# Optimization experiments

Measured on AMD Instinct MI355X. Metric: run time of the kernel, lower is better.

## Reference

```python
import jax, jax.numpy as jnp
import numpy as np

NEG_SLOPE = 0.2

def gat_conv(x, edge_index, W, a_src, a_dst, bias, heads, channels):
    # PyG GATConv (add_self_loops=False, dropout off in eval)
    N = x.shape[0]
    h = (x @ W).reshape(N, heads, channels)               # [N,H,C]
    src, dst = edge_index[0], edge_index[1]
    e_src = jnp.einsum('nhc,hc->nh', h, a_src)            # [N,H]
    e_dst = jnp.einsum('nhc,hc->nh', h, a_dst)
    e = jax.nn.leaky_relu(e_src[src] + e_dst[dst], NEG_SLOPE)  # [E,H]
    # softmax over incoming edges of each destination node
    m = jax.ops.segment_max(e, dst, num_segments=N)       # [N,H]
    ex = jnp.exp(e - m[dst])
    s = jax.ops.segment_sum(ex, dst, num_segments=N)
    alpha = ex / (s[dst] + 1e-16)                         # [E,H]
    msg = h[src] * alpha[:, :, None]                      # [E,H,C]
    out = jax.ops.segment_sum(msg, dst, num_segments=N)   # [N,H,C]
    return out.reshape(N, heads * channels) + bias


def setup_inputs() -> dict:
    key = jax.random.key(0)
    ks = jax.random.split(key, 12)
    N, E, SED, HID, H, F_OUT = 20000, 320000, 768, 128, 4, 128
    return {
        'x': jax.random.normal(ks[0], (N, SED), jnp.float32),
        'edge_index': jax.random.randint(ks[1], (2, E), 0, N, jnp.int32),
        'sentence_embedding': jax.random.normal(ks[2], (SED,), jnp.float32),
        'W1': jax.random.normal(ks[3], (2 * SED, H * HID), jnp.float32) * 0.02,
        'a1_src': jax.random.normal(ks[4], (H, HID), jnp.float32) * 0.1,
        'a1_dst': jax.random.normal(ks[5], (H, HID), jnp.float32) * 0.1,
        'b1': jax.random.normal(ks[6], (H * HID,), jnp.float32) * 0.02,
        'W2': jax.random.normal(ks[7], (H * HID, F_OUT), jnp.float32) * 0.02,
        'a2_src': jax.random.normal(ks[8], (1, F_OUT), jnp.float32) * 0.1,
        'a2_dst': jax.random.normal(ks[9], (1, F_OUT), jnp.float32) * 0.1,
        'b2': jax.random.normal(ks[10], (F_OUT,), jnp.float32) * 0.02,
    }


def reference(x, edge_index, sentence_embedding, W1, a1_src, a1_dst, b1, W2, a2_src, a2_dst, b2):
    N = x.shape[0]
    sent = jnp.broadcast_to(sentence_embedding[None, :], (N, sentence_embedding.shape[0]))
    h = jnp.concatenate([x, sent], axis=1)                # [N, 2*SED]
    h = gat_conv(h, edge_index, W1, a1_src, a1_dst, b1, heads=4, channels=128)
    h = jax.nn.elu(h)
    out = gat_conv(h, edge_index, W2, a2_src, a2_dst, b2, heads=1, channels=128)
    return out
```

## Files before the change

kernel.cpp:

```cpp
#include <hip/hip_runtime.h>
#include <cstdint>
#include <cstddef>

#define NSLOPE 0.2f

typedef __attribute__((ext_vector_type(8))) short bf16x8;
typedef __attribute__((ext_vector_type(4))) float f32x4;
typedef __attribute__((ext_vector_type(2))) float f32x2;
typedef unsigned short ushort_t;

__device__ inline ushort_t f2bf(float f) {
    union { float f; unsigned u; } v; v.f = f;
    unsigned u = v.u;
    unsigned r = (u + 0x7fffu + ((u >> 16) & 1u)) >> 16;
    return (ushort_t)r;
}
__device__ inline f32x2 unpack2(unsigned u) {
    union { unsigned u; float f; } lo, hi;
    lo.u = u << 16;
    hi.u = u & 0xffff0000u;
    f32x2 r; r.x = lo.f; r.y = hi.f;
    return r;
}
__device__ inline float leaky(float v) { return (v > 0.f) ? v : NSLOPE * v; }
__device__ inline float sel4(float4 q, bool b1, bool b2) {
    return b2 ? (b1 ? q.w : q.z) : (b1 ? q.y : q.x);
}

__global__ __launch_bounds__(256) void prep_kernel(
    const float* __restrict__ x, ushort_t* __restrict__ x_bf16, size_t nx,
    const float* __restrict__ W1, ushort_t* __restrict__ W1T,
    const float* __restrict__ W2, ushort_t* __restrict__ W2T,
    const float* __restrict__ sent, float* __restrict__ svec_part,
    int* __restrict__ indeg, int N, int nbCast, int nbZero)
{
    __shared__ float tile[32][33];
    int bid = blockIdx.x;
    int tid = threadIdx.x;
    if (bid < nbCast) {
        size_t i = ((size_t)bid * 256 + tid) * 8;
        if (i < nx) {
            float4 v0 = *(const float4*)(x + i);
            float4 v1 = *(const float4*)(x + i + 4);
            ushort_t r[8] = { f2bf(v0.x), f2bf(v0.y), f2bf(v0.z), f2bf(v0.w),
                              f2bf(v1.x), f2bf(v1.y), f2bf(v1.z), f2bf(v1.w) };
            *(uint4*)(x_bf16 + i) = *(uint4*)r;
        }
        return;
    }
    bid -= nbCast;
    if (bid < 384) {
        int k0 = (bid % 24) * 32, n0 = (bid / 24) * 32;
        int tx = tid & 31, ty = tid >> 5;
#pragma unroll
        for (int i = 0; i < 4; ++i)
            tile[ty + i * 8][tx] = W1[(size_t)(k0 + ty + i * 8) * 512 + n0 + tx];
        __syncthreads();
#pragma unroll
        for (int i = 0; i < 4; ++i)
            W1T[(size_t)(n0 + ty + i * 8) * 768 + k0 + tx] = f2bf(tile[tx][ty + i * 8]);
        return;
    }
    bid -= 384;
    if (bid < 64) {
        int k0 = (bid % 16) * 32, n0 = (bid / 16) * 32;
        int tx = tid & 31, ty = tid >> 5;
#pragma unroll
        for (int i = 0; i < 4; ++i)
            tile[ty + i * 8][tx] = W2[(size_t)(k0 + ty + i * 8) * 128 + n0 + tx];
        __syncthreads();
#pragma unroll
        for (int i = 0; i < 4; ++i)
            W2T[(size_t)(n0 + ty + i * 8) * 512 + k0 + tx] = f2bf(tile[tx][ty + i * 8]);
        return;
    }
    bid -= 64;
    if (bid < 16) {
        int cb = bid & 1, kb = bid >> 1;
        int c = cb * 256 + tid;
        int k0 = kb * 96;
        float acc = 0.f;
#pragma unroll 8
        for (int k = k0; k < k0 + 96; ++k)
            acc += sent[k] * W1[(size_t)(768 + k) * 512 + c];
        svec_part[kb * 512 + c] = acc;
        return;
    }
    bid -= 16;
    {
        int i = bid * 256 + tid;
        if (i < N) indeg[i] = 0;
    }
}

__device__ inline void async_copy16(const void* g, void* l) {
    __builtin_amdgcn_global_load_lds(
        (const __attribute__((address_space(1))) unsigned int*)g,
        (__attribute__((address_space(3))) unsigned int*)l, 16, 0, 0);
}

__global__ __launch_bounds__(256) void mfma_gemm_kernel(
    const ushort_t* __restrict__ A,
    const ushort_t* __restrict__ BT,
    const float* __restrict__ bias,
    ushort_t* __restrict__ Cb,
    const float* __restrict__ asrc,
    const float* __restrict__ adst,
    float* __restrict__ e_src,
    float* __restrict__ e_dst,
    int eStride,
    int M, int K, int Nc)
{
    __shared__ __align__(16) ushort_t lA[3][64 * 32];
    __shared__ __align__(16) ushort_t lB[3][128 * 32];
    __shared__ float e_lds[64][2][2];
    const int tid = threadIdx.x;
    const int wave = tid >> 6;
    const int lane = tid & 63;

    const int hh = blockIdx.y * gridDim.x + blockIdx.x;
    const int xcd = hh & 7;
    const int slot = hh >> 3;
    const int by = xcd + 8 * (slot / gridDim.x);
    const int bx = slot % gridDim.x;

    const int col0 = bx * 128;
    const int row0 = by * 64;
    const int wm = (wave & 1) * 32;
    const int wn = (wave >> 1) * 64;
    const int q = lane >> 4;
    const int ml = lane & 15;

    f32x4 acc[2][4] = {};

    const int rA = tid >> 2;
    const int gA = (tid & 3) ^ ((rA >> 1) & 3);
    int rowS[2], gS[2];
#pragma unroll
    for (int i = 0; i < 2; ++i) {
        int p = wave * 128 + i * 64 + lane;
        int r = p >> 2, s = p & 3;
        rowS[i] = r;
        gS[i] = s ^ ((r >> 1) & 3);
    }

    auto stage = [&](int k0, int buf) {
        {
            int ga = min(row0 + rA, M - 1);
            async_copy16(A + (size_t)ga * K + k0 + gA * 8,
                         &lA[buf][(size_t)(wave * 64) * 8]);
        }
#pragma unroll
        for (int i = 0; i < 2; ++i) {
            int pbs = wave * 128 + i * 64;
            async_copy16(BT + (size_t)(col0 + rowS[i]) * K + k0 + gS[i] * 8,
                         &lB[buf][(size_t)pbs * 8]);
        }
    };

    const int nt = K >> 5;
    stage(0, 0);
    if (nt > 1) {
        stage(32, 1);
        asm volatile("s_waitcnt vmcnt(3)\n\ts_barrier" ::: "memory");
    } else {
        asm volatile("s_waitcnt vmcnt(0)\n\ts_barrier" ::: "memory");
    }

    for (int t = 0; t < nt; ++t) {
        const int pb = t % 3;
        if (t + 2 < nt) stage((t + 2) << 5, (t + 2) % 3);
        bf16x8 af[2], bfr[4];
#pragma unroll
        for (int tt = 0; tt < 2; ++tt) {
            int m = wm + tt * 16 + ml;
            af[tt] = *(const bf16x8*)&lA[pb][(size_t)(m * 4 + (q ^ ((m >> 1) & 3))) * 8];
        }
#pragma unroll
        for (int tt = 0; tt < 4; ++tt) {
            int n = wn + tt * 16 + ml;
            bfr[tt] = *(const bf16x8*)&lB[pb][(size_t)(n * 4 + (q ^ ((n >> 1) & 3))) * 8];
        }
#pragma unroll
        for (int tm = 0; tm < 2; ++tm)
#pragma unroll
            for (int tn = 0; tn < 4; ++tn)
                acc[tm][tn] = __builtin_amdgcn_mfma_f32_16x16x32_bf16(
                    af[tm], bfr[tn], acc[tm][tn], 0, 0, 0);
        if (t + 2 < nt)
            asm volatile("s_waitcnt vmcnt(3) lgkmcnt(0)\n\ts_barrier" ::: "memory");
        else if (t + 1 < nt)
            asm volatile("s_waitcnt vmcnt(0) lgkmcnt(0)\n\ts_barrier" ::: "memory");
    }

    float es_acc[2][4] = {};
    float ed_acc[2][4] = {};
#pragma unroll
    for (int tm = 0; tm < 2; ++tm) {
        int rbase = row0 + wm + tm * 16 + q * 4;
#pragma unroll
        for (int tn = 0; tn < 4; ++tn) {
            int col = col0 + wn + tn * 16 + ml;
            float bb = bias ? bias[col] : 0.f;
            float av = asrc[col];
            float dv = adst[col];
#pragma unroll
            for (int r = 0; r < 4; ++r) {
                int row = rbase + r;
                float val = acc[tm][tn][r] + bb;
                if (row < M)
                    Cb[(size_t)row * Nc + col] = f2bf(val);
                es_acc[tm][r] += val * av;
                ed_acc[tm][r] += val * dv;
            }
        }
    }
    const int colhalf = wave >> 1;
#pragma unroll
    for (int tm = 0; tm < 2; ++tm) {
#pragma unroll
        for (int r = 0; r < 4; ++r) {
            float es = es_acc[tm][r], ed2 = ed_acc[tm][r];
#pragma unroll
            for (int st = 1; st < 16; st <<= 1) {
                es += __shfl_xor(es, st);
                ed2 += __shfl_xor(ed2, st);
            }
            if (ml == 0) {
                int rl = wm + tm * 16 + q * 4 + r;
                e_lds[rl][colhalf][0] = es;
                e_lds[rl][colhalf][1] = ed2;
            }
        }
    }
    __syncthreads();
    if (tid < 64) {
        int row = row0 + tid;
        if (row < M) {
            float es = e_lds[tid][0][0] + e_lds[tid][1][0];
            float ed2 = e_lds[tid][0][1] + e_lds[tid][1][1];
            e_src[(size_t)row * eStride + bx] = es;
            e_dst[(size_t)row * eStride + bx] = ed2;
        }
    }
}

__global__ void count_kernel(const int* __restrict__ ei, int* __restrict__ indeg, int E) {
    int e = blockIdx.x * blockDim.x + threadIdx.x;
    if (e < E) atomicAdd(&indeg[ei[E + e]], 1);
}

__global__ __launch_bounds__(1024) void scan_kernel(const int* __restrict__ indeg,
                                                    int* __restrict__ offsets,
                                                    int* __restrict__ cursor,
                                                    const float* __restrict__ svec_part,
                                                    float* __restrict__ svec, int N) {
    __shared__ int partial[1024];
    int tid = threadIdx.x;
    if (tid < 512) {
        float s = 0.f;
#pragma unroll
        for (int kb = 0; kb < 8; ++kb) s += svec_part[kb * 512 + tid];
        svec[tid] = s;
    }
    int per = (N + 1023) / 1024;
    int start = tid * per;
    int end = min(start + per, N);
    int sum = 0;
    if (start + per <= N && (per & 3) == 0) {
        for (int i = 0; i < per; i += 4) {
            int4 v = *(const int4*)(indeg + start + i);
            sum += v.x + v.y + v.z + v.w;
        }
    } else {
        for (int i = start; i < end; ++i) sum += indeg[i];
    }
    partial[tid] = sum;
    __syncthreads();
    for (int st = 1; st < 1024; st <<= 1) {
        int v = (tid >= st) ? partial[tid - st] : 0;
        __syncthreads();
        partial[tid] += v;
        __syncthreads();
    }
    int run = (tid == 0) ? 0 : partial[tid - 1];
    if (start + per <= N && (per & 3) == 0) {
        for (int i = 0; i < per; i += 4) {
            int4 v = *(const int4*)(indeg + start + i);
            int4 o;
            o.x = run;
            o.y = o.x + v.x;
            o.z = o.y + v.y;
            o.w = o.z + v.z;
            run = o.w + v.w;
            *(int4*)(offsets + start + i) = o;
            *(int4*)(cursor + start + i) = o;
        }
    } else {
        for (int i = start; i < end; ++i) {
            offsets[i] = run; cursor[i] = run;
            run += indeg[i];
        }
    }
    if (tid == 1023) offsets[N] = run;
}

__global__ void scatter_kernel(const int* __restrict__ ei, int* __restrict__ cursor,
                               int* __restrict__ csr_src, int E) {
    int e = blockIdx.x * blockDim.x + threadIdx.x;
    if (e < E) {
        int d = ei[E + e];
        int p = atomicAdd(&cursor[d], 1);
        csr_src[p] = ei[e];
    }
}

__global__ __launch_bounds__(256) void gather1_kernel(
    const ushort_t* __restrict__ h1b, const float* __restrict__ e_src,
    const float* __restrict__ e_dst, const int* __restrict__ offsets,
    const int* __restrict__ csr_src, const float* __restrict__ bias,
    ushort_t* __restrict__ outb, int N)
{
    const int lane = threadIdx.x & 63;
    const int wid0 = blockIdx.x * 4 + (threadIdx.x >> 6);
    const int nw = gridDim.x * 4;

    const int h = lane >> 4;
    const bool b1 = (h & 1), b2 = (h & 2);
    const ushort_t* hp = h1b + lane * 8;
    const int c = lane * 8;
    float bias0 = bias[c],     bias1 = bias[c + 1], bias2 = bias[c + 2],
          bias3 = bias[c + 3], bias4 = bias[c + 4], bias5 = bias[c + 5],
          bias6 = bias[c + 6], bias7 = bias[c + 7];

    for (int node = __builtin_amdgcn_readfirstlane(wid0); node < N;
         node = __builtin_amdgcn_readfirstlane(node + nw)) {
        int beg = offsets[node], end = offsets[node + 1];
        float4 ed = *(const float4*)&e_dst[node * 4];
        float edh = sel4(ed, b1, b2);

        f32x2 acc[4] = {};
        float s = 0.f;

        int j = beg;
        const int nb = (end - beg) >> 2;

        int4 ia, ib;
        float4 qa0, qa1, qa2, qa3, qb0, qb1, qb2, qb3;
        uint4 ua0, ua1, ua2, ua3, ub0, ub1, ub2, ub3;

        auto load4 = [&](int jj, int4& ix,
                         float4& q0, float4& q1, float4& q2, float4& q3,
                         uint4& u0, uint4& u1, uint4& u2, uint4& u3) {
            ix.x = csr_src[jj];     ix.y = csr_src[jj + 1];
            ix.z = csr_src[jj + 2]; ix.w = csr_src[jj + 3];
            q0 = *(const float4*)&e_src[ix.x * 4];
            q1 = *(const float4*)&e_src[ix.y * 4];
            q2 = *(const float4*)&e_src[ix.z * 4];
            q3 = *(const float4*)&e_src[ix.w * 4];
            u0 = *(const uint4*)&hp[(size_t)ix.x * 512];
            u1 = *(const uint4*)&hp[(size_t)ix.y * 512];
            u2 = *(const uint4*)&hp[(size_t)ix.z * 512];
            u3 = *(const uint4*)&hp[(size_t)ix.w * 512];
        };
        auto cons4 = [&](const float4& q0, const float4& q1,
                         const float4& q2, const float4& q3,
                         const uint4& u0, const uint4& u1,
                         const uint4& u2, const uint4& u3) {
            float w0 = __expf(leaky(sel4(q0, b1, b2) + edh));
            float w1 = __expf(leaky(sel4(q1, b1, b2) + edh));
            float w2 = __expf(leaky(sel4(q2, b1, b2) + edh));
            float w3 = __expf(leaky(sel4(q3, b1, b2) + edh));
            s += (w0 + w1) + (w2 + w3);
            f32x2 wv;
            wv.x = w0; wv.y = w0;
            acc[0] += unpack2(u0.x) * wv; acc[1] += unpack2(u0.y) * wv;
            acc[2] += unpack2(u0.z) * wv; acc[3] += unpack2(u0.w) * wv;
            wv.x = w1; wv.y = w1;
            acc[0] += unpack2(u1.x) * wv; acc[1] += unpack2(u1.y) * wv;
            acc[2] += unpack2(u1.z) * wv; acc[3] += unpack2(u1.w) * wv;
            wv.x = w2; wv.y = w2;
            acc[0] += unpack2(u2.x) * wv; acc[1] += unpack2(u2.y) * wv;
            acc[2] += unpack2(u2.z) * wv; acc[3] += unpack2(u2.w) * wv;
            wv.x = w3; wv.y = w3;
            acc[0] += unpack2(u3.x) * wv; acc[1] += unpack2(u3.y) * wv;
            acc[2] += unpack2(u3.z) * wv; acc[3] += unpack2(u3.w) * wv;
        };

        if (nb > 0) {
            load4(j, ia, qa0, qa1, qa2, qa3, ua0, ua1, ua2, ua3); j += 4;
            int b = 1;
            for (; b + 1 < nb; b += 2) {
                load4(j, ib, qb0, qb1, qb2, qb3, ub0, ub1, ub2, ub3); j += 4;
                cons4(qa0, qa1, qa2, qa3, ua0, ua1, ua2, ua3);
                load4(j, ia, qa0, qa1, qa2, qa3, ua0, ua1, ua2, ua3); j += 4;
                cons4(qb0, qb1, qb2, qb3, ub0, ub1, ub2, ub3);
            }
            if (b < nb) {
                load4(j, ib, qb0, qb1, qb2, qb3, ub0, ub1, ub2, ub3); j += 4;
                cons4(qa0, qa1, qa2, qa3, ua0, ua1, ua2, ua3);
                cons4(qb0, qb1, qb2, qb3, ub0, ub1, ub2, ub3);
            } else {
                cons4(qa0, qa1, qa2, qa3, ua0, ua1, ua2, ua3);
            }
        }
        for (; j < end; ++j) {
            int s0 = csr_src[j];
            float4 q0 = *(const float4*)&e_src[s0 * 4];
            float w0 = __expf(leaky(sel4(q0, b1, b2) + edh));
            s += w0;
            uint4 u0 = *(const uint4*)&hp[(size_t)s0 * 512];
            f32x2 wv; wv.x = w0; wv.y = w0;
            acc[0] += unpack2(u0.x) * wv; acc[1] += unpack2(u0.y) * wv;
            acc[2] += unpack2(u0.z) * wv; acc[3] += unpack2(u0.w) * wv;
        }
        float rs = 1.f / (s + 1e-16f);
        ushort_t o[8];
        float r0, r1;
        r0 = acc[0].x * rs + bias0; r1 = acc[0].y * rs + bias1;
        r0 = (r0 > 0.f) ? r0 : (__expf(r0) - 1.f);
        r1 = (r1 > 0.f) ? r1 : (__expf(r1) - 1.f);
        o[0] = f2bf(r0); o[1] = f2bf(r1);
        r0 = acc[1].x * rs + bias2; r1 = acc[1].y * rs + bias3;
        r0 = (r0 > 0.f) ? r0 : (__expf(r0) - 1.f);
        r1 = (r1 > 0.f) ? r1 : (__expf(r1) - 1.f);
        o[2] = f2bf(r0); o[3] = f2bf(r1);
        r0 = acc[2].x * rs + bias4; r1 = acc[2].y * rs + bias5;
        r0 = (r0 > 0.f) ? r0 : (__expf(r0) - 1.f);
        r1 = (r1 > 0.f) ? r1 : (__expf(r1) - 1.f);
        o[4] = f2bf(r0); o[5] = f2bf(r1);
        r0 = acc[3].x * rs + bias6; r1 = acc[3].y * rs + bias7;
        r0 = (r0 > 0.f) ? r0 : (__expf(r0) - 1.f);
        r1 = (r1 > 0.f) ? r1 : (__expf(r1) - 1.f);
        o[6] = f2bf(r0); o[7] = f2bf(r1);
        *(uint4*)&outb[(size_t)node * 512 + c] = *(uint4*)o;
    }
}

__global__ __launch_bounds__(256) void gather2_kernel(
    const ushort_t* __restrict__ h2b, const float* __restrict__ e_src,
    const float* __restrict__ e_dst, const int* __restrict__ offsets,
    const int* __restrict__ csr_src, const float* __restrict__ bias,
    float* __restrict__ out, int N)
{
    const int lane = threadIdx.x & 63;
    const int wid0 = blockIdx.x * 4 + (threadIdx.x >> 6);
    const int nw = gridDim.x * 4;

    const ushort_t* hp = h2b + lane * 2;
    float biasA = bias[lane * 2], biasB = bias[lane * 2 + 1];

    for (int node = __builtin_amdgcn_readfirstlane(wid0); node < N;
         node = __builtin_amdgcn_readfirstlane(node + nw)) {
        int beg = offsets[node], end = offsets[node + 1];
        float ed = e_dst[node];

        f32x2 acc = { 0.f, 0.f };
        float s = 0.f;

        int j = beg;
        const int nb = (end - beg) >> 2;

        int4 ia, ib;
        float fa0, fa1, fa2, fa3, fb0, fb1, fb2, fb3;
        unsigned ua0, ua1, ua2, ua3, ub0, ub1, ub2, ub3;

        auto load4 = [&](int jj, int4& ix,
                         float& f0, float& f1, float& f2, float& f3,
                         unsigned& u0, unsigned& u1, unsigned& u2, unsigned& u3) {
            ix.x = csr_src[jj];     ix.y = csr_src[jj + 1];
            ix.z = csr_src[jj + 2]; ix.w = csr_src[jj + 3];
            f0 = e_src[ix.x]; f1 = e_src[ix.y];
            f2 = e_src[ix.z]; f3 = e_src[ix.w];
            u0 = *(const unsigned*)&hp[(size_t)ix.x * 128];
            u1 = *(const unsigned*)&hp[(size_t)ix.y * 128];
            u2 = *(const unsigned*)&hp[(size_t)ix.z * 128];
            u3 = *(const unsigned*)&hp[(size_t)ix.w * 128];
        };
        auto cons4 = [&](float f0, float f1, float f2, float f3,
                         unsigned u0, unsigned u1, unsigned u2, unsigned u3) {
            float w0 = __expf(leaky(f0 + ed));
            float w1 = __expf(leaky(f1 + ed));
            float w2 = __expf(leaky(f2 + ed));
            float w3 = __expf(leaky(f3 + ed));
            s += (w0 + w1) + (w2 + w3);
            f32x2 w0v = { w0, w0 }, w1v = { w1, w1 }, w2v = { w2, w2 }, w3v = { w3, w3 };
            acc += unpack2(u0) * w0v;
            acc += unpack2(u1) * w1v;
            acc += unpack2(u2) * w2v;
            acc += unpack2(u3) * w3v;
        };

        if (nb > 0) {
            load4(j, ia, fa0, fa1, fa2, fa3, ua0, ua1, ua2, ua3); j += 4;
            int b = 1;
            for (; b + 1 < nb; b += 2) {
                load4(j, ib, fb0, fb1, fb2, fb3, ub0, ub1, ub2, ub3); j += 4;
                cons4(fa0, fa1, fa2, fa3, ua0, ua1, ua2, ua3);
                load4(j, ia, fa0, fa1, fa2, fa3, ua0, ua1, ua2, ua3); j += 4;
                cons4(fb0, fb1, fb2, fb3, ub0, ub1, ub2, ub3);
            }
            if (b < nb) {
                load4(j, ib, fb0, fb1, fb2, fb3, ub0, ub1, ub2, ub3); j += 4;
                cons4(fa0, fa1, fa2, fa3, ua0, ua1, ua2, ua3);
                cons4(fb0, fb1, fb2, fb3, ub0, ub1, ub2, ub3);
            } else {
                cons4(fa0, fa1, fa2, fa3, ua0, ua1, ua2, ua3);
            }
        }
        for (; j < end; ++j) {
            int s0 = csr_src[j];
            float w0 = __expf(leaky(e_src[s0] + ed));
            s += w0;
            unsigned u0 = *(const unsigned*)&hp[(size_t)s0 * 128];
            f32x2 w0v = { w0, w0 };
            acc += unpack2(u0) * w0v;
        }
        float rs = 1.f / (s + 1e-16f);
        float2 o = make_float2(acc.x * rs + biasA, acc.y * rs + biasB);
        *(float2*)&out[(size_t)node * 128 + lane * 2] = o;
    }
}

extern "C" void kernel_launch(void* const* d_in, const int* in_sizes, int n_in,
                              void* d_out, int out_size, void* d_ws, size_t ws_size,
                              hipStream_t stream) {
    const float* x      = (const float*)d_in[0];
    const int*   ei     = (const int*)  d_in[1];
    const float* sent   = (const float*)d_in[2];
    const float* W1     = (const float*)d_in[3];
    const float* a1_src = (const float*)d_in[4];
    const float* a1_dst = (const float*)d_in[5];
    const float* b1     = (const float*)d_in[6];
    const float* W2     = (const float*)d_in[7];
    const float* a2_src = (const float*)d_in[8];
    const float* a2_dst = (const float*)d_in[9];
    const float* b2     = (const float*)d_in[10];
    float* out = (float*)d_out;

    const int N = in_sizes[0] / 768;
    const int E = in_sizes[1] / 2;

    char* p = (char*)d_ws;
    auto carve = [&](size_t bytes) {
        char* q = p;
        p += (bytes + 255) & ~(size_t)255;
        return q;
    };
    ushort_t* h1b = (ushort_t*)carve((size_t)N * 512 * 2);
    char* shared_region = carve((size_t)N * 768 * 2);
    ushort_t* x_bf16 = (ushort_t*)shared_region;
    ushort_t* h_elu_b = (ushort_t*)shared_region;
    ushort_t* h2b = (ushort_t*)carve((size_t)N * 128 * 2);
    ushort_t* W1T = (ushort_t*)carve((size_t)512 * 768 * 2);
    ushort_t* W2T = (ushort_t*)carve((size_t)128 * 512 * 2);
    float* svec_part = (float*)carve(8 * 512 * 4);
    float* svec   = (float*)carve(512 * 4);
    float* e_src1 = (float*)carve((size_t)N * 4 * 4);
    float* e_dst1 = (float*)carve((size_t)N * 4 * 4);
    float* e_src2 = (float*)carve((size_t)N * 4);
    float* e_dst2 = (float*)carve((size_t)N * 4);
    int*   indeg  = (int*)carve((size_t)N * 4);
    int*   offs   = (int*)carve((size_t)(N + 1) * 4);
    int*   cursor = (int*)carve((size_t)N * 4);
    int*   csrsrc = (int*)carve((size_t)E * 4);

    size_t nx = (size_t)N * 768;
    int nbCast = (int)((nx / 8 + 255) / 256);
    int nbZero = (N + 255) / 256;
    int nbPrep = nbCast + 384 + 64 + 16 + nbZero;

    prep_kernel<<<nbPrep, 256, 0, stream>>>(x, x_bf16, nx, W1, W1T, W2, W2T,
                                            sent, svec_part, indeg, N, nbCast, nbZero);
    count_kernel<<<(E + 255) / 256, 256, 0, stream>>>(ei, indeg, E);
    scan_kernel<<<1, 1024, 0, stream>>>(indeg, offs, cursor, svec_part, svec, N);
    scatter_kernel<<<(E + 255) / 256, 256, 0, stream>>>(ei, cursor, csrsrc, E);

    int nyPad = (((N + 63) / 64) + 7) & ~7;

    mfma_gemm_kernel<<<dim3(4, nyPad), 256, 0, stream>>>(
        x_bf16, W1T, svec, h1b, a1_src, a1_dst, e_src1, e_dst1, 4, N, 768, 512);

    gather1_kernel<<<2048, 256, 0, stream>>>(
        h1b, e_src1, e_dst1, offs, csrsrc, b1, h_elu_b, N);

    mfma_gemm_kernel<<<dim3(1, nyPad), 256, 0, stream>>>(
        h_elu_b, W2T, nullptr, h2b, a2_src, a2_dst, e_src2, e_dst2, 1, N, 512, 128);

    gather2_kernel<<<2048, 256, 0, stream>>>(
        h2b, e_src2, e_dst2, offs, csrsrc, b2, out, N);
}
```

Before: 282.8 us.

## Merge prep, count, scan, scatter into one cooperative kernel with grid syncs

Replaces the four preprocessing launches (cast/transpose prep, indegree count, single-block scan, CSR scatter) with one cooperative kernel of 1024 blocks that separates the phases with grid.sync(). The scan becomes a two-level block-sum scan distributed across the grid instead of one 1024-thread block. The goal is to remove launch gaps and the serial single-block scan. In exchange it adds five grid-wide barriers, a serial per-block offset write done by thread 0, and the svec reduction is now 2 blocks doing a 768-long loop. It also depends on all 1024 blocks being co-resident.

```diff
diff --git a/kernel.cpp b/kernel.cpp
--- a/kernel.cpp
+++ b/kernel.cpp
@@ -1,8 +1,12 @@
 #include <hip/hip_runtime.h>
+#include <hip/hip_cooperative_groups.h>
 #include <cstdint>
 #include <cstddef>
 
+namespace cg = cooperative_groups;
+
 #define NSLOPE 0.2f
+#define BUILD_NB 1024
 
 typedef __attribute__((ext_vector_type(8))) short bf16x8;
 typedef __attribute__((ext_vector_type(4))) float f32x4;
@@ -27,69 +31,133 @@
     return b2 ? (b1 ? q.w : q.z) : (b1 ? q.y : q.x);
 }
 
-__global__ __launch_bounds__(256) void prep_kernel(
+__global__ __launch_bounds__(256, 4) void build_kernel(
     const float* __restrict__ x, ushort_t* __restrict__ x_bf16, size_t nx,
     const float* __restrict__ W1, ushort_t* __restrict__ W1T,
     const float* __restrict__ W2, ushort_t* __restrict__ W2T,
-    const float* __restrict__ sent, float* __restrict__ svec_part,
-    int* __restrict__ indeg, int N, int nbCast, int nbZero)
+    const float* __restrict__ sent, float* __restrict__ svec,
+    const int* __restrict__ ei, int E,
+    int* __restrict__ indeg, int* __restrict__ offsets,
+    int* __restrict__ cursor, int* __restrict__ csr_src,
+    int* __restrict__ blockSums, int N)
 {
+    cg::grid_group grid = cg::this_grid();
     __shared__ float tile[32][33];
-    int bid = blockIdx.x;
-    int tid = threadIdx.x;
-    if (bid < nbCast) {
-        size_t i = ((size_t)bid * 256 + tid) * 8;
-        if (i < nx) {
+    __shared__ int sdata[256];
+    const int tid = threadIdx.x;
+    const int bid = blockIdx.x;
+    const size_t gsize = (size_t)BUILD_NB * 256;
+
+    if (bid < 384) {
+        int k0 = (bid % 24) * 32, n0 = (bid / 24) * 32;
+        int tx = tid & 31, ty = tid >> 5;
+#pragma unroll
+        for (int i = 0; i < 4; ++i)
+            tile[ty + i * 8][tx] = W1[(size_t)(k0 + ty + i * 8) * 512 + n0 + tx];
+        __syncthreads();
+#pragma unroll
+        for (int i = 0; i < 4; ++i)
+            W1T[(size_t)(n0 + ty + i * 8) * 768 + k0 + tx] = f2bf(tile[tx][ty + i * 8]);
+    } else if (bid < 448) {
+        int b2 = bid - 384;
+        int k0 = (b2 % 16) * 32, n0 = (b2 / 16) * 32;
+        int tx = tid & 31, ty = tid >> 5;
+#pragma unroll
+        for (int i = 0; i < 4; ++i)
+            tile[ty + i * 8][tx] = W2[(size_t)(k0 + ty + i * 8) * 128 + n0 + tx];
+        __syncthreads();
+#pragma unroll
+        for (int i = 0; i < 4; ++i)
+            W2T[(size_t)(n0 + ty + i * 8) * 512 + k0 + tx] = f2bf(tile[tx][ty + i * 8]);
+    } else if (bid < 450) {
+        int c = (bid - 448) * 256 + tid;
+        float acc = 0.f;
+#pragma unroll 8
+        for (int k = 0; k < 768; ++k)
+            acc += sent[k] * W1[(size_t)(768 + k) * 512 + c];
+        svec[c] = acc;
+    }
+    {
+        size_t nvec = nx >> 3;
+        for (size_t v = (size_t)bid * 256 + tid; v < nvec; v += gsize) {
+            size_t i = v * 8;
             float4 v0 = *(const float4*)(x + i);
             float4 v1 = *(const float4*)(x + i + 4);
             ushort_t r[8] = { f2bf(v0.x), f2bf(v0.y), f2bf(v0.z), f2bf(v0.w),
                               f2bf(v1.x), f2bf(v1.y), f2bf(v1.z), f2bf(v1.w) };
             *(uint4*)(x_bf16 + i) = *(uint4*)r;
         }
-        return;
-    }
-    bid -= nbCast;
-    if (bid < 384) {
-        int k0 = (bid % 24) * 32, n0 = (bid / 24) * 32;
-        int tx = tid & 31, ty = tid >> 5;
-#pragma unroll
-        for (int i = 0; i < 4; ++i)
-            tile[ty + i * 8][tx] = W1[(size_t)(k0 + ty + i * 8) * 512 + n0 + tx];
+    }
+    for (int i = bid * 256 + tid; i < N; i += (int)gsize) indeg[i] = 0;
+
+    grid.sync();
+
+    for (int e = bid * 256 + tid; e < E; e += (int)gsize)
+        atomicAdd(&indeg[ei[E + e]], 1);
+
+    grid.sync();
+
+    const int per = (N + BUILD_NB - 1) / BUILD_NB;
+    const int start = bid * per;
+    const int endn = min(start + per, N);
+    {
+        int v = 0;
+        for (int i = start + tid; i < endn; i += 256) v += indeg[i];
+        sdata[tid] = v;
         __syncthreads();
-#pragma unroll
-        for (int i = 0; i < 4; ++i)
-            W1T[(size_t)(n0 + ty + i * 8) * 768 + k0 + tx] = f2bf(tile[tx][ty + i * 8]);
-        return;
-    }
-    bid -= 384;
-    if (bid < 64) {
-        int k0 = (bid % 16) * 32, n0 = (bid / 16) * 32;
-        int tx = tid & 31, ty = tid >> 5;
-#pragma unroll
-        for (int i = 0; i < 4; ++i)
-            tile[ty + i * 8][tx] = W2[(size_t)(k0 + ty + i * 8) * 128 + n0 + tx];
+        for (int st = 128; st >= 1; st >>= 1) {
+            if (tid < st) sdata[tid] += sdata[tid + st];
+            __syncthreads();
+        }
+        if (tid == 0) blockSums[bid] = sdata[0];
+    }
+
+    grid.sync();
+
+    if (bid == 0) {
+        int loc[BUILD_NB / 256];
+        int base = tid * (BUILD_NB / 256);
+        int sum = 0;
+#pragma unroll
+        for (int i = 0; i < BUILD_NB / 256; ++i) {
+            loc[i] = blockSums[base + i];
+            sum += loc[i];
+        }
+        sdata[tid] = sum;
         __syncthreads();
-#pragma unroll
-        for (int i = 0; i < 4; ++i)
-            W2T[(size_t)(n0 + ty + i * 8) * 512 + k0 + tx] = f2bf(tile[tx][ty + i * 8]);
-        return;
-    }
-    bid -= 64;
-    if (bid < 16) {
-        int cb = bid & 1, kb = bid >> 1;
-        int c = cb * 256 + tid;
-        int k0 = kb * 96;
-        float acc = 0.f;
-#pragma unroll 8
-        for (int k = k0; k < k0 + 96; ++k)
-            acc += sent[k] * W1[(size_t)(768 + k) * 512 + c];
-        svec_part[kb * 512 + c] = acc;
-        return;
-    }
-    bid -= 16;
-    {
-        int i = bid * 256 + tid;
-        if (i < N) indeg[i] = 0;
+        for (int st = 1; st < 256; st <<= 1) {
+            int val = (tid >= st) ? sdata[tid - st] : 0;
+            __syncthreads();
+            sdata[tid] += val;
+            __syncthreads();
+        }
+        int run = (tid == 0) ? 0 : sdata[tid - 1];
+#pragma unroll
+        for (int i = 0; i < BUILD_NB / 256; ++i) {
+            int t = loc[i];
+            blockSums[base + i] = run;
+            run += t;
+        }
+    }
+
+    grid.sync();
+
+    if (tid == 0 && start < N) {
+        int run = blockSums[bid];
+        for (int i = start; i < endn; ++i) {
+            offsets[i] = run;
+            cursor[i] = run;
+            run += indeg[i];
+        }
+        if (endn == N) offsets[N] = run;
+    }
+
+    grid.sync();
+
+    for (int e = bid * 256 + tid; e < E; e += (int)gsize) {
+        int d = ei[E + e];
+        int p = atomicAdd(&cursor[d], 1);
+        csr_src[p] = ei[e];
     }
 }
 
@@ -242,76 +310,6 @@
             e_src[(size_t)row * eStride + bx] = es;
             e_dst[(size_t)row * eStride + bx] = ed2;
         }
-    }
-}
-
-__global__ void count_kernel(const int* __restrict__ ei, int* __restrict__ indeg, int E) {
-    int e = blockIdx.x * blockDim.x + threadIdx.x;
-    if (e < E) atomicAdd(&indeg[ei[E + e]], 1);
-}
-
-__global__ __launch_bounds__(1024) void scan_kernel(const int* __restrict__ indeg,
-                                                    int* __restrict__ offsets,
-                                                    int* __restrict__ cursor,
-                                                    const float* __restrict__ svec_part,
-                                                    float* __restrict__ svec, int N) {
-    __shared__ int partial[1024];
-    int tid = threadIdx.x;
-    if (tid < 512) {
-        float s = 0.f;
-#pragma unroll
-        for (int kb = 0; kb < 8; ++kb) s += svec_part[kb * 512 + tid];
-        svec[tid] = s;
-    }
-    int per = (N + 1023) / 1024;
-    int start = tid * per;
-    int end = min(start + per, N);
-    int sum = 0;
-    if (start + per <= N && (per & 3) == 0) {
-        for (int i = 0; i < per; i += 4) {
-            int4 v = *(const int4*)(indeg + start + i);
-            sum += v.x + v.y + v.z + v.w;
-        }
-    } else {
-        for (int i = start; i < end; ++i) sum += indeg[i];
-    }
-    partial[tid] = sum;
-    __syncthreads();
-    for (int st = 1; st < 1024; st <<= 1) {
-        int v = (tid >= st) ? partial[tid - st] : 0;
-        __syncthreads();
-        partial[tid] += v;
-        __syncthreads();
-    }
-    int run = (tid == 0) ? 0 : partial[tid - 1];
-    if (start + per <= N && (per & 3) == 0) {
-        for (int i = 0; i < per; i += 4) {
-            int4 v = *(const int4*)(indeg + start + i);
-            int4 o;
-            o.x = run;
-            o.y = o.x + v.x;
-            o.z = o.y + v.y;
-            o.w = o.z + v.z;
-            run = o.w + v.w;
-            *(int4*)(offsets + start + i) = o;
-            *(int4*)(cursor + start + i) = o;
-        }
-    } else {
-        for (int i = start; i < end; ++i) {
-            offsets[i] = run; cursor[i] = run;
-            run += indeg[i];
-        }
-    }
-    if (tid == 1023) offsets[N] = run;
-}
-
-__global__ void scatter_kernel(const int* __restrict__ ei, int* __restrict__ cursor,
-                               int* __restrict__ csr_src, int E) {
-    int e = blockIdx.x * blockDim.x + threadIdx.x;
-    if (e < E) {
-        int d = ei[E + e];
-        int p = atomicAdd(&cursor[d], 1);
-        csr_src[p] = ei[e];
     }
 }
 
@@ -554,7 +552,6 @@
     ushort_t* h2b = (ushort_t*)carve((size_t)N * 128 * 2);
     ushort_t* W1T = (ushort_t*)carve((size_t)512 * 768 * 2);
     ushort_t* W2T = (ushort_t*)carve((size_t)128 * 512 * 2);
-    float* svec_part = (float*)carve(8 * 512 * 4);
     float* svec   = (float*)carve(512 * 4);
     float* e_src1 = (float*)carve((size_t)N * 4 * 4);
     float* e_dst1 = (float*)carve((size_t)N * 4 * 4);
@@ -564,17 +561,19 @@
     int*   offs   = (int*)carve((size_t)(N + 1) * 4);
     int*   cursor = (int*)carve((size_t)N * 4);
     int*   csrsrc = (int*)carve((size_t)E * 4);
+    int*   blockSums = (int*)carve(BUILD_NB * 4);
 
     size_t nx = (size_t)N * 768;
-    int nbCast = (int)((nx / 8 + 255) / 256);
-    int nbZero = (N + 255) / 256;
-    int nbPrep = nbCast + 384 + 64 + 16 + nbZero;
-
-    prep_kernel<<<nbPrep, 256, 0, stream>>>(x, x_bf16, nx, W1, W1T, W2, W2T,
-                                            sent, svec_part, indeg, N, nbCast, nbZero);
-    count_kernel<<<(E + 255) / 256, 256, 0, stream>>>(ei, indeg, E);
-    scan_kernel<<<1, 1024, 0, stream>>>(indeg, offs, cursor, svec_part, svec, N);
-    scatter_kernel<<<(E + 255) / 256, 256, 0, stream>>>(ei, cursor, csrsrc, E);
+    int E_ = E, N_ = N;
+
+    void* bargs[] = { (void*)&x, (void*)&x_bf16, (void*)&nx,
+                      (void*)&W1, (void*)&W1T, (void*)&W2, (void*)&W2T,
+                      (void*)&sent, (void*)&svec,
+                      (void*)&ei, (void*)&E_,
+                      (void*)&indeg, (void*)&offs, (void*)&cursor,
+                      (void*)&csrsrc, (void*)&blockSums, (void*)&N_ };
+    hipLaunchCooperativeKernel((void*)build_kernel, dim3(BUILD_NB), dim3(256),
+                               bargs, 0, stream);
 
     int nyPad = (((N + 63) / 64) + 7) & ~7;
 
```

Result: slower. 922.1 us (+226.0%).

## Shard layer-1 gather across 8 column slices per block group

Applied to the files above, without the earlier changes.

The layer-1 gather kernel now splits each node's 512 output columns into 8 shards selected by blockIdx, so each wave handles 64 columns with one bf16 element per lane instead of the full row with 8 elements per lane. The intent is to raise parallelism and cut per-thread register pressure by dropping the hand-written software pipeline. In exchange, each edge's index and attention score are loaded and exponentiated 8 times (once per shard), and h loads shrink to 2-byte scalar accesses, which may waste memory transactions. Behaviour depends on the grid size being a multiple of 8, which is set in host code that is not shown.

```diff
diff --git a/kernel.cpp b/kernel.cpp
--- a/kernel.cpp
+++ b/kernel.cpp
@@ -14,6 +14,10 @@
     unsigned u = v.u;
     unsigned r = (u + 0x7fffu + ((u >> 16) & 1u)) >> 16;
     return (ushort_t)r;
+}
+__device__ inline float bf2f(ushort_t u) {
+    union { unsigned u; float f; } v; v.u = ((unsigned)u) << 16;
+    return v.f;
 }
 __device__ inline f32x2 unpack2(unsigned u) {
     union { unsigned u; float f; } lo, hi;
@@ -23,9 +27,6 @@
     return r;
 }
 __device__ inline float leaky(float v) { return (v > 0.f) ? v : NSLOPE * v; }
-__device__ inline float sel4(float4 q, bool b1, bool b2) {
-    return b2 ? (b1 ? q.w : q.z) : (b1 ? q.y : q.x);
-}
 
 __global__ __launch_bounds__(256) void prep_kernel(
     const float* __restrict__ x, ushort_t* __restrict__ x_bf16, size_t nx,
@@ -322,118 +323,43 @@
     ushort_t* __restrict__ outb, int N)
 {
     const int lane = threadIdx.x & 63;
-    const int wid0 = blockIdx.x * 4 + (threadIdx.x >> 6);
-    const int nw = gridDim.x * 4;
-
-    const int h = lane >> 4;
-    const bool b1 = (h & 1), b2 = (h & 2);
-    const ushort_t* hp = h1b + lane * 8;
-    const int c = lane * 8;
-    float bias0 = bias[c],     bias1 = bias[c + 1], bias2 = bias[c + 2],
-          bias3 = bias[c + 3], bias4 = bias[c + 4], bias5 = bias[c + 5],
-          bias6 = bias[c + 6], bias7 = bias[c + 7];
-
-    for (int node = __builtin_amdgcn_readfirstlane(wid0); node < N;
-         node = __builtin_amdgcn_readfirstlane(node + nw)) {
+    const int shard = blockIdx.x & 7;
+    const int wsub = __builtin_amdgcn_readfirstlane(
+        (blockIdx.x >> 3) * 4 + (threadIdx.x >> 6));
+    const int nWsub = (gridDim.x >> 3) * 4;
+    const int c = shard * 64 + lane;
+    const int h = shard >> 1;
+    const float bc = bias[c];
+    const ushort_t* hp = h1b + c;
+
+    for (int node = wsub; node < N; node += nWsub) {
         int beg = offsets[node], end = offsets[node + 1];
-        float4 ed = *(const float4*)&e_dst[node * 4];
-        float edh = sel4(ed, b1, b2);
-
-        f32x2 acc[4] = {};
-        float s = 0.f;
-
+        float ed = e_dst[node * 4 + h];
+        float acc = 0.f, s = 0.f;
         int j = beg;
-        const int nb = (end - beg) >> 2;
-
-        int4 ia, ib;
-        float4 qa0, qa1, qa2, qa3, qb0, qb1, qb2, qb3;
-        uint4 ua0, ua1, ua2, ua3, ub0, ub1, ub2, ub3;
-
-        auto load4 = [&](int jj, int4& ix,
-                         float4& q0, float4& q1, float4& q2, float4& q3,
-                         uint4& u0, uint4& u1, uint4& u2, uint4& u3) {
-            ix.x = csr_src[jj];     ix.y = csr_src[jj + 1];
-            ix.z = csr_src[jj + 2]; ix.w = csr_src[jj + 3];
-            q0 = *(const float4*)&e_src[ix.x * 4];
-            q1 = *(const float4*)&e_src[ix.y * 4];
-            q2 = *(const float4*)&e_src[ix.z * 4];
-            q3 = *(const float4*)&e_src[ix.w * 4];
-            u0 = *(const uint4*)&hp[(size_t)ix.x * 512];
-            u1 = *(const uint4*)&hp[(size_t)ix.y * 512];
-            u2 = *(const uint4*)&hp[(size_t)ix.z * 512];
-            u3 = *(const uint4*)&hp[(size_t)ix.w * 512];
-        };
-        auto cons4 = [&](const float4& q0, const float4& q1,
-                         const float4& q2, const float4& q3,
-                         const uint4& u0, const uint4& u1,
-                         const uint4& u2, const uint4& u3) {
-            float w0 = __expf(leaky(sel4(q0, b1, b2) + edh));
-            float w1 = __expf(leaky(sel4(q1, b1, b2) + edh));
-            float w2 = __expf(leaky(sel4(q2, b1, b2) + edh));
-            float w3 = __expf(leaky(sel4(q3, b1, b2) + edh));
+        for (; j + 4 <= end; j += 4) {
+            int s0 = csr_src[j],     s1 = csr_src[j + 1];
+            int s2 = csr_src[j + 2], s3 = csr_src[j + 3];
+            float w0 = __expf(leaky(e_src[s0 * 4 + h] + ed));
+            float w1 = __expf(leaky(e_src[s1 * 4 + h] + ed));
+            float w2 = __expf(leaky(e_src[s2 * 4 + h] + ed));
+            float w3 = __expf(leaky(e_src[s3 * 4 + h] + ed));
             s += (w0 + w1) + (w2 + w3);
-            f32x2 wv;
-            wv.x = w0; wv.y = w0;
-            acc[0] += unpack2(u0.x) * wv; acc[1] += unpack2(u0.y) * wv;
-            acc[2] += unpack2(u0.z) * wv; acc[3] += unpack2(u0.w) * wv;
-            wv.x = w1; wv.y = w1;
-            acc[0] += unpack2(u1.x) * wv; acc[1] += unpack2(u1.y) * wv;
-            acc[2] += unpack2(u1.z) * wv; acc[3] += unpack2(u1.w) * wv;
-            wv.x = w2; wv.y = w2;
-            acc[0] += unpack2(u2.x) * wv; acc[1] += unpack2(u2.y) * wv;
-            acc[2] += unpack2(u2.z) * wv; acc[3] += unpack2(u2.w) * wv;
-            wv.x = w3; wv.y = w3;
-            acc[0] += unpack2(u3.x) * wv; acc[1] += unpack2(u3.y) * wv;
-            acc[2] += unpack2(u3.z) * wv; acc[3] += unpack2(u3.w) * wv;
-        };
-
-        if (nb > 0) {
-            load4(j, ia, qa0, qa1, qa2, qa3, ua0, ua1, ua2, ua3); j += 4;
-            int b = 1;
-            for (; b + 1 < nb; b += 2) {
-                load4(j, ib, qb0, qb1, qb2, qb3, ub0, ub1, ub2, ub3); j += 4;
-                cons4(qa0, qa1, qa2, qa3, ua0, ua1, ua2, ua3);
-                load4(j, ia, qa0, qa1, qa2, qa3, ua0, ua1, ua2, ua3); j += 4;
-                cons4(qb0, qb1, qb2, qb3, ub0, ub1, ub2, ub3);
-            }
-            if (b < nb) {
-                load4(j, ib, qb0, qb1, qb2, qb3, ub0, ub1, ub2, ub3); j += 4;
-                cons4(qa0, qa1, qa2, qa3, ua0, ua1, ua2, ua3);
-                cons4(qb0, qb1, qb2, qb3, ub0, ub1, ub2, ub3);
-            } else {
-                cons4(qa0, qa1, qa2, qa3, ua0, ua1, ua2, ua3);
-            }
+            float v0 = bf2f(hp[(size_t)s0 * 512]);
+            float v1 = bf2f(hp[(size_t)s1 * 512]);
+            float v2 = bf2f(hp[(size_t)s2 * 512]);
+            float v3 = bf2f(hp[(size_t)s3 * 512]);
+            acc += w0 * v0 + w1 * v1 + w2 * v2 + w3 * v3;
         }
         for (; j < end; ++j) {
             int s0 = csr_src[j];
-            float4 q0 = *(const float4*)&e_src[s0 * 4];
-            float w0 = __expf(leaky(sel4(q0, b1, b2) + edh));
+            float w0 = __expf(leaky(e_src[s0 * 4 + h] + ed));
             s += w0;
-            uint4 u0 = *(const uint4*)&hp[(size_t)s0 * 512];
-            f32x2 wv; wv.x = w0; wv.y = w0;
-            acc[0] += unpack2(u0.x) * wv; acc[1] += unpack2(u0.y) * wv;
-            acc[2] += unpack2(u0.z) * wv; acc[3] += unpack2(u0.w) * wv;
-        }
-        float rs = 1.f / (s + 1e-16f);
-        ushort_t o[8];
-        float r0, r1;
-        r0 = acc[0].x * rs + bias0; r1 = acc[0].y * rs + bias1;
-        r0 = (r0 > 0.f) ? r0 : (__expf(r0) - 1.f);
-        r1 = (r1 > 0.f) ? r1 : (__expf(r1) - 1.f);
-        o[0] = f2bf(r0); o[1] = f2bf(r1);
-        r0 = acc[1].x * rs + bias2; r1 = acc[1].y * rs + bias3;
-        r0 = (r0 > 0.f) ? r0 : (__expf(r0) - 1.f);
-        r1 = (r1 > 0.f) ? r1 : (__expf(r1) - 1.f);
-        o[2] = f2bf(r0); o[3] = f2bf(r1);
-        r0 = acc[2].x * rs + bias4; r1 = acc[2].y * rs + bias5;
-        r0 = (r0 > 0.f) ? r0 : (__expf(r0) - 1.f);
-        r1 = (r1 > 0.f) ? r1 : (__expf(r1) - 1.f);
-        o[4] = f2bf(r0); o[5] = f2bf(r1);
-        r0 = acc[3].x * rs + bias6; r1 = acc[3].y * rs + bias7;
-        r0 = (r0 > 0.f) ? r0 : (__expf(r0) - 1.f);
-        r1 = (r1 > 0.f) ? r1 : (__expf(r1) - 1.f);
-        o[6] = f2bf(r0); o[7] = f2bf(r1);
-        *(uint4*)&outb[(size_t)node * 512 + c] = *(uint4*)o;
+            acc += w0 * bf2f(hp[(size_t)s0 * 512]);
+        }
+        float r = acc / (s + 1e-16f) + bc;
+        r = (r > 0.f) ? r : (__expf(r) - 1.f);
+        outb[(size_t)node * 512 + c] = f2bf(r);
     }
 }
 
```

After: 331.9 us. 17.4% more time.
